# Kernel optimization log

Hardware: AMD Instinct MI355X
Metric: run time of the kernel (lower is better)

Reference implementation:

```python
import jax, jax.numpy as jnp
import numpy as np

N_NODES = 50000   # total nodes across all graphs in the batch
N_EDGES = 800000  # avg degree 16
F_IN = 64         # input_dim
HID = 128         # hidden_dim
N_GRAPHS = 500    # number of graphs (max batch id)
N_CLS = 10        # output_dim
MLP_HID = 50      # post_mp hidden width (hard-coded in module)


def setup_inputs() -> dict:
    key = jax.random.key(0)
    ks = jax.random.split(key, 11)
    x = jax.random.normal(ks[0], (N_NODES, F_IN), dtype=jnp.float32)
    edge_index = jax.random.randint(ks[1], (2, N_EDGES), 0, N_NODES, dtype=jnp.int64)
    batch = jnp.sort(jax.random.randint(ks[2], (N_NODES,), 0, N_GRAPHS, dtype=jnp.int64))
    # SAGEConv params (lin_l on aggregated neighbors, lin_r root weight)
    W_neigh = jax.random.normal(ks[3], (F_IN, HID), dtype=jnp.float32) / np.sqrt(F_IN)
    W_self = jax.random.normal(ks[4], (F_IN, HID), dtype=jnp.float32) / np.sqrt(F_IN)
    b = jax.random.normal(ks[5], (HID,), dtype=jnp.float32) * 0.01
    # post_mp: Linear(HID,50) -> ReLU -> Linear(50, N_CLS)
    W1 = jax.random.normal(ks[6], (HID, MLP_HID), dtype=jnp.float32) / np.sqrt(HID)
    b1 = jax.random.normal(ks[7], (MLP_HID,), dtype=jnp.float32) * 0.01
    W2 = jax.random.normal(ks[8], (MLP_HID, N_CLS), dtype=jnp.float32) / np.sqrt(MLP_HID)
    b2 = jax.random.normal(ks[9], (N_CLS,), dtype=jnp.float32) * 0.01
    return {"x": x, "edge_index": edge_index, "batch": batch,
            "W_neigh": W_neigh, "W_self": W_self, "b": b,
            "W1": W1, "b1": b1, "W2": W2, "b2": b2}


def reference(x, edge_index, batch, W_neigh, W_self, b, W1, b1, W2, b2):
    src, dst = edge_index[0], edge_index[1]
    # SAGEConv: mean-aggregate neighbor features, then linear + root weight
    agg = jax.ops.segment_sum(x[src], dst, num_segments=N_NODES)          # [N, F_IN]
    deg = jax.ops.segment_sum(jnp.ones((src.shape[0], 1), x.dtype), dst,
                              num_segments=N_NODES)                       # [N, 1]
    agg = agg / jnp.maximum(deg, 1.0)
    emb = agg @ W_neigh + x @ W_self + b                                  # [N, HID]
    h = jax.nn.relu(emb)
    # global mean pool over graphs
    pooled = jax.ops.segment_sum(h, batch, num_segments=N_GRAPHS)         # [G, HID]
    cnt = jax.ops.segment_sum(jnp.ones((h.shape[0], 1), h.dtype), batch,
                              num_segments=N_GRAPHS)                      # [G, 1]
    pooled = pooled / jnp.maximum(cnt, 1.0)
    # post_mp MLP + log_softmax
    logits = jax.nn.relu(pooled @ W1 + b1) @ W2 + b2                      # [G, N_CLS]
    return emb, jax.nn.log_softmax(logits, axis=1)
```

## Files before the change

### kernel.cpp

```cpp
#include <hip/hip_runtime.h>

#define N_NODES_C 50000
#define F_IN_C 64
#define HID_C 128
#define N_GRAPHS_C 500
#define N_CLS_C 10
#define MLP_HID_C 50
#define SCAN_TILE 1024
#define N_SCAN_BLK ((N_NODES_C + SCAN_TILE - 1) / SCAN_TILE)
#define N_TILES (N_NODES_C / 16)
#define N_RANGES 8
#define RANGE_SZ (N_NODES_C / N_RANGES)
#define S_STRIPES 64

using short8 = __attribute__((ext_vector_type(8))) short;
using f32x4  = __attribute__((ext_vector_type(4))) float;

__device__ __forceinline__ int bl_i(int v, int l) {
    return __builtin_amdgcn_readlane(v, l);
}
__device__ __forceinline__ float uf(unsigned u) { return __uint_as_float(u); }

__device__ __forceinline__ unsigned pk_bf16(float a, float b) {
    unsigned ua = __float_as_uint(a), ub = __float_as_uint(b);
    ua += 0x7FFFu + ((ua >> 16) & 1u);
    ub += 0x7FFFu + ((ub >> 16) & 1u);
    return (ua >> 16) | (ub & 0xFFFF0000u);
}

union U8 { unsigned u[4]; uint4 q; short8 s; };

__global__ __launch_bounds__(256) void prep_kernel(
    const float* __restrict__ x,
    const int* __restrict__ batch,
    unsigned* __restrict__ xh,
    int* __restrict__ start)
{
    int tid = blockIdx.x * 256 + threadIdx.x;
    int stride = gridDim.x * 256;
    const float2* xf2 = (const float2*)x;
    int nx = N_NODES_C * (F_IN_C / 2);
    for (int i = tid; i < nx; i += stride) {
        float2 v = xf2[i];
        xh[i] = pk_bf16(v.x, v.y);
    }
    for (int i = tid; i < N_NODES_C; i += stride) {
        int b = batch[i];
        if (i == 0) { for (int g = 0; g <= b; ++g) start[g] = 0; }
        else { int p = batch[i - 1]; for (int g = p + 1; g <= b; ++g) start[g] = i; }
        if (i == N_NODES_C - 1) { for (int g = b + 1; g <= N_GRAPHS_C; ++g) start[g] = N_NODES_C; }
    }
}

__global__ __launch_bounds__(1024) void hist2d_kernel(
    const int* __restrict__ dst, int* __restrict__ h, int n_edges, int stripe)
{
    __shared__ int lh[RANGE_SZ];
    int s = blockIdx.x >> 3, r = blockIdx.x & 7;
    int lo = r * RANGE_SZ;
    int t = threadIdx.x;
    for (int i = t; i < RANGE_SZ; i += 1024) lh[i] = 0;
    __syncthreads();
    int e1 = min(n_edges, (s + 1) * stripe);
    for (int e = s * stripe + t; e < e1; e += 1024) {
        int d = dst[e] - lo;
        if ((unsigned)d < (unsigned)RANGE_SZ) atomicAdd(&lh[d], 1);
    }
    __syncthreads();
    for (int i = t; i < RANGE_SZ; i += 1024)
        h[(size_t)s * N_NODES_C + lo + i] = lh[i];
}

__global__ __launch_bounds__(256) void reduce_kernel(
    const int* __restrict__ h, int* __restrict__ p, int* __restrict__ deg_i)
{
    int n = blockIdx.x * 256 + threadIdx.x;
    if (n >= N_NODES_C) return;
    int run = 0;
    #pragma unroll 8
    for (int s = 0; s < S_STRIPES; ++s) {
        int c = h[(size_t)s * N_NODES_C + n];
        p[(size_t)s * N_NODES_C + n] = run;
        run += c;
    }
    deg_i[n] = run;
}

__global__ __launch_bounds__(256) void scan1_kernel(
    const int* __restrict__ deg_i, int* __restrict__ bsums, int n)
{
    __shared__ int s[256];
    int base = blockIdx.x * SCAN_TILE;
    int t = threadIdx.x;
    int sum = 0;
    #pragma unroll
    for (int j = 0; j < 4; ++j) {
        int i = base + t * 4 + j;
        sum += (i < n) ? deg_i[i] : 0;
    }
    s[t] = sum;
    __syncthreads();
    for (int off = 128; off > 0; off >>= 1) {
        if (t < off) s[t] += s[t + off];
        __syncthreads();
    }
    if (t == 0) bsums[blockIdx.x] = s[0];
}

__global__ __launch_bounds__(256) void scan3_kernel(
    const int* __restrict__ deg_i, const int* __restrict__ bsums,
    int* __restrict__ off, int n)
{
    __shared__ int s[256];
    __shared__ int sbp;
    int b = blockIdx.x;
    int t = threadIdx.x;
    if (t < 64) {
        int v = (t < b) ? bsums[t] : 0;
        #pragma unroll
        for (int m = 1; m < 64; m <<= 1) v += __shfl_xor(v, m, 64);
        if (t == 0) sbp = v;
    }
    int base = b * SCAN_TILE;
    int v4[4];
    int sum = 0;
    #pragma unroll
    for (int j = 0; j < 4; ++j) {
        int i = base + t * 4 + j;
        v4[j] = (i < n) ? deg_i[i] : 0;
        sum += v4[j];
    }
    s[t] = sum;
    __syncthreads();
    for (int o = 1; o < 256; o <<= 1) {
        int tmp = (t >= o) ? s[t - o] : 0;
        __syncthreads();
        s[t] += tmp;
        __syncthreads();
    }
    int run = s[t] - sum + sbp;
    #pragma unroll
    for (int j = 0; j < 4; ++j) {
        int i = base + t * 4 + j;
        if (i < n) off[i] = run;
        run += v4[j];
    }
    if (b == N_SCAN_BLK - 1 && t == 255) off[n] = sbp + s[255];
}

__global__ __launch_bounds__(1024) void scatter2d_kernel(
    const int* __restrict__ src, const int* __restrict__ dst,
    const int* __restrict__ off, const int* __restrict__ p,
    int* __restrict__ adj, int n_edges, int stripe)
{
    __shared__ int lcur[RANGE_SZ];
    int s = blockIdx.x >> 3, r = blockIdx.x & 7;
    int lo = r * RANGE_SZ;
    int t = threadIdx.x;
    for (int i = t; i < RANGE_SZ; i += 1024)
        lcur[i] = off[lo + i] + p[(size_t)s * N_NODES_C + lo + i];
    __syncthreads();
    int e1 = min(n_edges, (s + 1) * stripe);
    for (int e = s * stripe + t; e < e1; e += 1024) {
        int d = dst[e] - lo;
        if ((unsigned)d < (unsigned)RANGE_SZ) {
            int pos = atomicAdd(&lcur[d], 1);
            adj[pos] = src[e];
        }
    }
}

__global__ __launch_bounds__(256) void gather_mean_kernel(
    const unsigned* __restrict__ xh,
    const int* __restrict__ adj,
    const int* __restrict__ off,
    unsigned* __restrict__ agg)
{
    int t = threadIdx.x;
    int wave = t >> 6, lane = t & 63;
    int node = blockIdx.x * 4 + wave;
    int o = off[node];
    int d = off[node + 1] - o;
    int half = lane >> 5;
    int col = lane & 31;
    float sx = 0.f, sy = 0.f;

    for (int j0 = 0; j0 < d; j0 += 64) {
        int c = d - j0; if (c > 64) c = 64;
        int nid = (lane < c) ? adj[o + j0 + lane] : 0;
        int j = 0;
        for (; j + 8 <= c; j += 8) {
            #pragma unroll
            for (int m = 0; m < 4; ++m) {
                int re = bl_i(nid, j + 2 * m);
                int ro = bl_i(nid, j + 2 * m + 1);
                int row = half ? ro : re;
                unsigned u = xh[(size_t)row * 32 + col];
                sx += uf(u << 16); sy += uf(u & 0xFFFF0000u);
            }
        }
        for (; j < c; j += 2) {
            int re = bl_i(nid, j);
            int ro = (j + 1 < c) ? bl_i(nid, j + 1) : re;
            int row = half ? ro : re;
            unsigned u = xh[(size_t)row * 32 + col];
            if (half && j + 1 >= c) u = 0u;
            sx += uf(u << 16); sy += uf(u & 0xFFFF0000u);
        }
    }
    sx += __shfl_xor(sx, 32, 64);
    sy += __shfl_xor(sy, 32, 64);
    if (half == 0) {
        float inv = 1.0f / fmaxf((float)d, 1.0f);
        agg[(size_t)node * 32 + col] = pk_bf16(sx * inv, sy * inv);
    }
}

__global__ __launch_bounds__(256) void gemm_kernel(
    const unsigned* __restrict__ xh,
    const unsigned* __restrict__ agg,
    const float* __restrict__ Wn,
    const float* __restrict__ Ws,
    const float* __restrict__ bias,
    float* __restrict__ emb_out)
{
    __shared__ unsigned sWk[64 * 129];
    __shared__ float sb[128];
    int t = threadIdx.x;
    for (int e = t; e < 64 * 128; e += 256) {
        int kk = e >> 7, n = e & 127;
        float w0, w1;
        if (kk < 32) { w0 = Ws[(2 * kk) * 128 + n];      w1 = Ws[(2 * kk + 1) * 128 + n]; }
        else         { w0 = Wn[(2 * kk - 64) * 128 + n]; w1 = Wn[(2 * kk - 63) * 128 + n]; }
        sWk[kk * 129 + n] = pk_bf16(w0, w1);
    }
    if (t < 128) sb[t] = bias[t];
    __syncthreads();

    int wave = t >> 6, lane = t & 63;
    int lr = lane & 15, lg = lane >> 4;
    int tile = blockIdx.x * 4 + wave;
    if (tile >= N_TILES) return;

    const uint4* xr = (const uint4*)(xh + ((size_t)tile * 16 + lr) * 32);
    const uint4* ar = (const uint4*)(agg + ((size_t)tile * 16 + lr) * 32);
    U8 A[4];
    A[0].q = xr[lg];
    A[1].q = xr[4 + lg];
    A[2].q = ar[lg];
    A[3].q = ar[4 + lg];

    #pragma unroll
    for (int c = 0; c < 8; ++c) {
        float bv = sb[c * 16 + lr];
        f32x4 acc = {bv, bv, bv, bv};
        #pragma unroll
        for (int s = 0; s < 4; ++s) {
            U8 B;
            #pragma unroll
            for (int jj = 0; jj < 4; ++jj)
                B.u[jj] = sWk[(16 * s + 4 * lg + jj) * 129 + c * 16 + lr];
            acc = __builtin_amdgcn_mfma_f32_16x16x32_bf16(A[s].s, B.s, acc, 0, 0, 0);
        }
        #pragma unroll
        for (int r = 0; r < 4; ++r)
            emb_out[((size_t)tile * 16 + lg * 4 + r) * 128 + c * 16 + lr] = acc[r];
    }
}

__global__ __launch_bounds__(256) void poolhead_kernel(
    const float* __restrict__ emb, const int* __restrict__ start,
    const float* __restrict__ W1, const float* __restrict__ b1,
    const float* __restrict__ W2, const float* __restrict__ b2,
    float* __restrict__ logits_out)
{
    int g = blockIdx.x;
    int t = threadIdx.x;
    __shared__ float sp[HID_C];
    __shared__ float shid[MLP_HID_C];
    __shared__ float sl[N_CLS_C];
    __shared__ float4 red[256];

    int s0 = start[g], e0 = start[g + 1];
    int q = t & 31, r0 = t >> 5;
    const float4* e4 = (const float4*)emb;
    float4 acc = make_float4(0.f, 0.f, 0.f, 0.f);
    for (int r = s0 + r0; r < e0; r += 8) {
        float4 v = e4[(size_t)r * 32 + q];
        acc.x += fmaxf(v.x, 0.f); acc.y += fmaxf(v.y, 0.f);
        acc.z += fmaxf(v.z, 0.f); acc.w += fmaxf(v.w, 0.f);
    }
    red[t] = acc;
    __syncthreads();
    if (t < 32) {
        float4 a = red[t];
        #pragma unroll
        for (int r = 1; r < 8; ++r) {
            float4 b = red[t + 32 * r];
            a.x += b.x; a.y += b.y; a.z += b.z; a.w += b.w;
        }
        float inv = 1.0f / fmaxf((float)(e0 - s0), 1.0f);
        ((float4*)sp)[t] = make_float4(a.x * inv, a.y * inv, a.z * inv, a.w * inv);
    }
    __syncthreads();

    if (t < MLP_HID_C) {
        float a = b1[t];
        #pragma unroll 8
        for (int k = 0; k < HID_C; ++k) a += sp[k] * W1[k * MLP_HID_C + t];
        shid[t] = fmaxf(a, 0.0f);
    }
    __syncthreads();

    if (t < N_CLS_C) {
        float a = b2[t];
        #pragma unroll
        for (int k = 0; k < MLP_HID_C; ++k) a += shid[k] * W2[k * N_CLS_C + t];
        sl[t] = a;
    }
    __syncthreads();

    if (t < N_CLS_C) {
        float m = sl[0];
        #pragma unroll
        for (int i = 1; i < N_CLS_C; ++i) m = fmaxf(m, sl[i]);
        float sum = 0.0f;
        #pragma unroll
        for (int i = 0; i < N_CLS_C; ++i) sum += expf(sl[i] - m);
        logits_out[(size_t)g * N_CLS_C + t] = sl[t] - m - logf(sum);
    }
}

extern "C" void kernel_launch(void* const* d_in, const int* in_sizes, int n_in,
                              void* d_out, int out_size, void* d_ws, size_t ws_size,
                              hipStream_t stream) {
    const float* x      = (const float*)d_in[0];
    const int*   ei     = (const int*)d_in[1];
    const int*   batch  = (const int*)d_in[2];
    const float* Wn     = (const float*)d_in[3];
    const float* Ws     = (const float*)d_in[4];
    const float* bias   = (const float*)d_in[5];
    const float* W1     = (const float*)d_in[6];
    const float* b1     = (const float*)d_in[7];
    const float* W2     = (const float*)d_in[8];
    const float* b2     = (const float*)d_in[9];

    float* out = (float*)d_out;
    int n_edges = in_sizes[1] / 2;
    const int* src = ei;
    const int* dst = ei + n_edges;
    int stripe = (n_edges + S_STRIPES - 1) / S_STRIPES;

    int* deg_i   = (int*)d_ws;
    int* off     = deg_i + N_NODES_C;
    int* bsums   = off + (N_NODES_C + 1);
    int* start   = bsums + 64;
    unsigned* xh = (unsigned*)(start + (N_GRAPHS_C + 1) + 2);
    int* adj     = (int*)(xh + (size_t)N_NODES_C * 32);
    unsigned* agg = (unsigned*)(adj + ((n_edges + 3) & ~3));
    int* h       = (int*)(agg + (size_t)N_NODES_C * 32);
    int* p       = h + (size_t)S_STRIPES * N_NODES_C;

    prep_kernel<<<1024, 256, 0, stream>>>(x, batch, xh, start);
    hist2d_kernel<<<S_STRIPES * N_RANGES, 1024, 0, stream>>>(dst, h, n_edges, stripe);
    reduce_kernel<<<(N_NODES_C + 255) / 256, 256, 0, stream>>>(h, p, deg_i);
    scan1_kernel<<<N_SCAN_BLK, 256, 0, stream>>>(deg_i, bsums, N_NODES_C);
    scan3_kernel<<<N_SCAN_BLK, 256, 0, stream>>>(deg_i, bsums, off, N_NODES_C);
    scatter2d_kernel<<<S_STRIPES * N_RANGES, 1024, 0, stream>>>(src, dst, off, p,
                                                                adj, n_edges, stripe);

    gather_mean_kernel<<<12500, 256, 0, stream>>>(xh, adj, off, agg);

    gemm_kernel<<<782, 256, 0, stream>>>(xh, agg, Wn, Ws, bias, out);

    poolhead_kernel<<<N_GRAPHS_C, 256, 0, stream>>>(out, start, W1, b1, W2, b2,
                                                    out + (size_t)N_NODES_C * HID_C);
}
```

Measured before the change: 94.16 us.

## Fuse degree reduce with block sums and gather two nodes per wave

Merges scan1 into the per-node stripe reduce kernel, which now runs with 1024-thread blocks and writes per-block sums directly, removing one launch. The gather kernel now processes two nodes per wave with 16 independent loads in flight. It pads neighbor lists with a zero row appended to xh, which removes the tail branch. This raises memory-level parallelism in the gather. The cost is that reduce runs on only 49 blocks, and the wave's trip count follows the larger of the two degrees, so the shorter node pads up to 16-edge granularity.

```diff
diff --git a/kernel.cpp b/kernel.cpp
--- a/kernel.cpp
+++ b/kernel.cpp
@@ -12,6 +12,7 @@
 #define N_RANGES 8
 #define RANGE_SZ (N_NODES_C / N_RANGES)
 #define S_STRIPES 64
+#define ZROW N_NODES_C
 
 using short8 = __attribute__((ext_vector_type(8))) short;
 using f32x4  = __attribute__((ext_vector_type(4))) float;
@@ -40,9 +41,10 @@
     int stride = gridDim.x * 256;
     const float2* xf2 = (const float2*)x;
     int nx = N_NODES_C * (F_IN_C / 2);
-    for (int i = tid; i < nx; i += stride) {
-        float2 v = xf2[i];
-        xh[i] = pk_bf16(v.x, v.y);
+    int total = (N_NODES_C + 1) * (F_IN_C / 2);
+    for (int i = tid; i < total; i += stride) {
+        if (i < nx) { float2 v = xf2[i]; xh[i] = pk_bf16(v.x, v.y); }
+        else        xh[i] = 0u;
     }
     for (int i = tid; i < N_NODES_C; i += stride) {
         int b = batch[i];
@@ -71,40 +73,30 @@
         h[(size_t)s * N_NODES_C + lo + i] = lh[i];
 }
 
-__global__ __launch_bounds__(256) void reduce_kernel(
-    const int* __restrict__ h, int* __restrict__ p, int* __restrict__ deg_i)
-{
-    int n = blockIdx.x * 256 + threadIdx.x;
-    if (n >= N_NODES_C) return;
+__global__ __launch_bounds__(1024) void reduce_kernel(
+    const int* __restrict__ h, int* __restrict__ p, int* __restrict__ deg_i,
+    int* __restrict__ bsums)
+{
+    __shared__ int sred[1024];
+    int t = threadIdx.x;
+    int n = blockIdx.x * 1024 + t;
     int run = 0;
-    #pragma unroll 8
-    for (int s = 0; s < S_STRIPES; ++s) {
-        int c = h[(size_t)s * N_NODES_C + n];
-        p[(size_t)s * N_NODES_C + n] = run;
-        run += c;
-    }
-    deg_i[n] = run;
-}
-
-__global__ __launch_bounds__(256) void scan1_kernel(
-    const int* __restrict__ deg_i, int* __restrict__ bsums, int n)
-{
-    __shared__ int s[256];
-    int base = blockIdx.x * SCAN_TILE;
-    int t = threadIdx.x;
-    int sum = 0;
-    #pragma unroll
-    for (int j = 0; j < 4; ++j) {
-        int i = base + t * 4 + j;
-        sum += (i < n) ? deg_i[i] : 0;
-    }
-    s[t] = sum;
-    __syncthreads();
-    for (int off = 128; off > 0; off >>= 1) {
-        if (t < off) s[t] += s[t + off];
+    if (n < N_NODES_C) {
+        #pragma unroll 8
+        for (int s = 0; s < S_STRIPES; ++s) {
+            int c = h[(size_t)s * N_NODES_C + n];
+            p[(size_t)s * N_NODES_C + n] = run;
+            run += c;
+        }
+        deg_i[n] = run;
+    }
+    sred[t] = (n < N_NODES_C) ? run : 0;
+    __syncthreads();
+    for (int o = 512; o > 0; o >>= 1) {
+        if (t < o) sred[t] += sred[t + o];
         __syncthreads();
     }
-    if (t == 0) bsums[blockIdx.x] = s[0];
+    if (t == 0) bsums[blockIdx.x] = sred[0];
 }
 
 __global__ __launch_bounds__(256) void scan3_kernel(
@@ -178,41 +170,55 @@
 {
     int t = threadIdx.x;
     int wave = t >> 6, lane = t & 63;
-    int node = blockIdx.x * 4 + wave;
-    int o = off[node];
-    int d = off[node + 1] - o;
-    int half = lane >> 5;
-    int col = lane & 31;
-    float sx = 0.f, sy = 0.f;
-
-    for (int j0 = 0; j0 < d; j0 += 64) {
-        int c = d - j0; if (c > 64) c = 64;
-        int nid = (lane < c) ? adj[o + j0 + lane] : 0;
-        int j = 0;
-        for (; j + 8 <= c; j += 8) {
-            #pragma unroll
-            for (int m = 0; m < 4; ++m) {
-                int re = bl_i(nid, j + 2 * m);
-                int ro = bl_i(nid, j + 2 * m + 1);
+    int base = (blockIdx.x * 4 + wave) * 2;
+    int n0 = base, n1 = base + 1;
+    int o0 = off[n0], m0 = off[n0 + 1], e1v = off[n1 + 1];
+    int d0 = m0 - o0;
+    int o1 = m0, d1 = e1v - m0;
+    int half = lane >> 5, col = lane & 31;
+    float sx0 = 0.f, sy0 = 0.f, sx1 = 0.f, sy1 = 0.f;
+
+    int dm = max(d0, d1);
+    for (int j0 = 0; j0 < dm; j0 += 64) {
+        int c0 = min(max(d0 - j0, 0), 64);
+        int c1 = min(max(d1 - j0, 0), 64);
+        int nid0 = (lane < c0) ? adj[o0 + j0 + lane] : ZROW;
+        int nid1 = (lane < c1) ? adj[o1 + j0 + lane] : ZROW;
+        int cm = max(c0, c1);
+        for (int j = 0; j < cm; j += 16) {
+            unsigned u[16];
+            #pragma unroll
+            for (int m = 0; m < 8; ++m) {
+                int re = bl_i(nid0, j + 2 * m);
+                int ro = bl_i(nid0, j + 2 * m + 1);
                 int row = half ? ro : re;
-                unsigned u = xh[(size_t)row * 32 + col];
-                sx += uf(u << 16); sy += uf(u & 0xFFFF0000u);
+                u[m] = xh[(size_t)row * 32 + col];
             }
-        }
-        for (; j < c; j += 2) {
-            int re = bl_i(nid, j);
-            int ro = (j + 1 < c) ? bl_i(nid, j + 1) : re;
-            int row = half ? ro : re;
-            unsigned u = xh[(size_t)row * 32 + col];
-            if (half && j + 1 >= c) u = 0u;
-            sx += uf(u << 16); sy += uf(u & 0xFFFF0000u);
-        }
-    }
-    sx += __shfl_xor(sx, 32, 64);
-    sy += __shfl_xor(sy, 32, 64);
+            #pragma unroll
+            for (int m = 0; m < 8; ++m) {
+                int re = bl_i(nid1, j + 2 * m);
+                int ro = bl_i(nid1, j + 2 * m + 1);
+                int row = half ? ro : re;
+                u[8 + m] = xh[(size_t)row * 32 + col];
+            }
+            #pragma unroll
+            for (int m = 0; m < 8; ++m) {
+                sx0 += uf(u[m] << 16); sy0 += uf(u[m] & 0xFFFF0000u);
+            }
+            #pragma unroll
+            for (int m = 0; m < 8; ++m) {
+                sx1 += uf(u[8 + m] << 16); sy1 += uf(u[8 + m] & 0xFFFF0000u);
+            }
+        }
+    }
+    sx0 += __shfl_xor(sx0, 32, 64); sy0 += __shfl_xor(sy0, 32, 64);
+    sx1 += __shfl_xor(sx1, 32, 64); sy1 += __shfl_xor(sy1, 32, 64);
     if (half == 0) {
-        float inv = 1.0f / fmaxf((float)d, 1.0f);
-        agg[(size_t)node * 32 + col] = pk_bf16(sx * inv, sy * inv);
+        float inv = 1.0f / fmaxf((float)d0, 1.0f);
+        agg[(size_t)n0 * 32 + col] = pk_bf16(sx0 * inv, sy0 * inv);
+    } else {
+        float inv = 1.0f / fmaxf((float)d1, 1.0f);
+        agg[(size_t)n1 * 32 + col] = pk_bf16(sx1 * inv, sy1 * inv);
     }
 }
 
@@ -356,20 +362,19 @@
     int* bsums   = off + (N_NODES_C + 1);
     int* start   = bsums + 64;
     unsigned* xh = (unsigned*)(start + (N_GRAPHS_C + 1) + 2);
-    int* adj     = (int*)(xh + (size_t)N_NODES_C * 32);
+    int* adj     = (int*)(xh + (size_t)(N_NODES_C + 1) * 32);
     unsigned* agg = (unsigned*)(adj + ((n_edges + 3) & ~3));
     int* h       = (int*)(agg + (size_t)N_NODES_C * 32);
     int* p       = h + (size_t)S_STRIPES * N_NODES_C;
 
     prep_kernel<<<1024, 256, 0, stream>>>(x, batch, xh, start);
     hist2d_kernel<<<S_STRIPES * N_RANGES, 1024, 0, stream>>>(dst, h, n_edges, stripe);
-    reduce_kernel<<<(N_NODES_C + 255) / 256, 256, 0, stream>>>(h, p, deg_i);
-    scan1_kernel<<<N_SCAN_BLK, 256, 0, stream>>>(deg_i, bsums, N_NODES_C);
+    reduce_kernel<<<N_SCAN_BLK, 1024, 0, stream>>>(h, p, deg_i, bsums);
     scan3_kernel<<<N_SCAN_BLK, 256, 0, stream>>>(deg_i, bsums, off, N_NODES_C);
     scatter2d_kernel<<<S_STRIPES * N_RANGES, 1024, 0, stream>>>(src, dst, off, p,
                                                                 adj, n_edges, stripe);
 
-    gather_mean_kernel<<<12500, 256, 0, stream>>>(xh, adj, off, agg);
+    gather_mean_kernel<<<6250, 256, 0, stream>>>(xh, adj, off, agg);
 
     gemm_kernel<<<782, 256, 0, stream>>>(xh, agg, Wn, Ws, bias, out);
 
```

Result: no change. 94.75 us (+0.6%).
